# Performance work log

Measured on AMD Instinct MI355X. Metric: run time of the kernel, lower is better.

The kernel has to match this reference:

```python
import jax, jax.numpy as jnp
import numpy as np

B, Q, D = 262144, 25, 9  # batch, num_queries, key_value_size
SEGS = [(0, 3), (3, 13), (13, 23), (23, 25)]  # joint, object, goal, block token ranges
EPS = 1e-5


def setup_inputs() -> dict:
    key = jax.random.key(0)
    ks = jax.random.split(key, 17)
    inp = {"x": jax.random.normal(ks[0], (B, Q, D), dtype=jnp.float32)}
    names = ["W_jk", "b_jk", "W_ok", "b_ok", "W_gk", "b_gk", "W_bk", "b_bk",
             "W_jv", "b_jv", "W_ov", "b_ov", "W_gv", "b_gv", "W_bv", "b_bv"]
    scale = 1.0 / np.sqrt(D)  # torch Linear default init range
    for i, n in enumerate(names):
        shp = (D, D) if n.startswith("W") else (D,)
        inp[n] = jax.random.uniform(ks[i + 1], shp, jnp.float32, -scale, scale)
    inp["ln_g"] = jnp.ones((D,), jnp.float32)
    inp["ln_b"] = jnp.zeros((D,), jnp.float32)
    return inp


def reference(x, W_jk, b_jk, W_ok, b_ok, W_gk, b_gk, W_bk, b_bk,
              W_jv, b_jv, W_ov, b_ov, W_gv, b_gv, W_bv, b_bv, ln_g, ln_b):
    def proj(seg, W, b):
        s, e = seg  # [B, n, D] @ W.T + b  (torch Linear convention: W is [out,in])
        return jnp.einsum('bnd,kd->bnk', x[:, s:e], W) + b

    keys = jnp.concatenate([proj(SEGS[0], W_jk, b_jk), proj(SEGS[1], W_ok, b_ok),
                            proj(SEGS[2], W_gk, b_gk), proj(SEGS[3], W_bk, b_bk)], axis=1)
    values = jnp.concatenate([proj(SEGS[0], W_jv, b_jv), proj(SEGS[1], W_ov, b_ov),
                              proj(SEGS[2], W_gv, b_gv), proj(SEGS[3], W_bv, b_bv)], axis=1)
    # self-attention with queries == keys (as in the original forward)
    scores = jnp.einsum('bqd,bkd->bqk', keys, keys)  # [B, Q, Q]
    attn = jax.nn.softmax(scores, axis=-1)  # dropout = identity in eval
    res = jnp.einsum('bqk,bkd->bqd', attn, values)
    y = x + res
    mu = jnp.mean(y, axis=-1, keepdims=True)
    var = jnp.mean(jnp.square(y - mu), axis=-1, keepdims=True)
    return (y - mu) * jax.lax.rsqrt(var + EPS) * ln_g + ln_b
```

## Files before the change

### kernel.cpp

```cpp
#include <hip/hip_runtime.h>

#define TPB 256
#define BPB 64
#define NQ 25
#define ND 9
#define XWORDS (BPB * NQ * ND)
#define X4 (XWORDS / 4)
#define KV_OFF 8000
#define SMEM_WORDS 16000
#define SOFTMAX_SHIFT 40.0f

typedef _Float16 h2 __attribute__((ext_vector_type(2)));
typedef float f4 __attribute__((ext_vector_type(4)));

__device__ __forceinline__ float dot2acc(h2 a, h2 b, float c) {
#if __has_builtin(__builtin_amdgcn_fdot2)
    return __builtin_amdgcn_fdot2(a, b, c, false);
#else
    return c + (float)a[0] * (float)b[0] + (float)a[1] * (float)b[1];
#endif
}

__global__ __launch_bounds__(TPB, 2) void attn_fused(
    const float* __restrict__ x,
    const float* __restrict__ Wjk, const float* __restrict__ bjk,
    const float* __restrict__ Wok, const float* __restrict__ bok,
    const float* __restrict__ Wgk, const float* __restrict__ bgk,
    const float* __restrict__ Wbk, const float* __restrict__ bbk,
    const float* __restrict__ Wjv, const float* __restrict__ bjv,
    const float* __restrict__ Wov, const float* __restrict__ bov,
    const float* __restrict__ Wgv, const float* __restrict__ bgv,
    const float* __restrict__ Wbv, const float* __restrict__ bbv,
    const float* __restrict__ ln_g, const float* __restrict__ ln_b,
    float* __restrict__ out)
{
    __shared__ unsigned int sm[SMEM_WORDS];

    const int tid  = threadIdx.x;
    const int lane = tid & 63;
    const int w    = __builtin_amdgcn_readfirstlane(tid >> 6);
    const long base = (long)blockIdx.x * XWORDS;

    {
        const f4* src = (const f4*)(x + base);
        f4* dst = (f4*)sm;
        #pragma unroll
        for (int i = 0; i < 15; ++i) {
            int idx = tid + i * TPB;
            if (idx < X4) dst[idx] = src[idx];
        }
    }
    __syncthreads();

    const int qs = (w == 0) ? 0 : 6 * w + 1;
    const int qc = (w == 0) ? 7 : 6;

    float xr[7][9];
    #pragma unroll
    for (int j = 0; j < 7; ++j) {
        if (j < qc) {
            const float* xsrc = (const float*)sm + lane * (NQ * ND) + (qs + j) * ND;
            #pragma unroll
            for (int d = 0; d < ND; ++d) xr[j][d] = xsrc[d];
        }
    }
    __syncthreads();

    h2 kreg[7][5];
    #pragma unroll
    for (int j = 0; j < 7; ++j) {
        if (j < qc) {
            const int q = qs + j;
            const int seg = (q >= 3) + (q >= 13) + (q >= 23);
            const float* Wk = (seg == 0) ? Wjk : (seg == 1) ? Wok : (seg == 2) ? Wgk : Wbk;
            const float* bk = (seg == 0) ? bjk : (seg == 1) ? bok : (seg == 2) ? bgk : bbk;
            const float* Wv = (seg == 0) ? Wjv : (seg == 1) ? Wov : (seg == 2) ? Wgv : Wbv;
            const float* bv = (seg == 0) ? bjv : (seg == 1) ? bov : (seg == 2) ? bgv : bbv;

            float kk[9], vv[9];
            #pragma unroll
            for (int o = 0; o < ND; ++o) {
                float ak = bk[o];
                float av = bv[o];
                #pragma unroll
                for (int i = 0; i < ND; ++i) {
                    ak += Wk[o * ND + i] * xr[j][i];
                    av += Wv[o * ND + i] * xr[j][i];
                }
                kk[o] = ak; vv[o] = av;
            }
            #pragma unroll
            for (int hp = 0; hp < 5; ++hp) {
                float k0 = kk[2 * hp], k1 = (hp < 4) ? kk[2 * hp + 1] : 0.0f;
                float v0 = vv[2 * hp], v1 = (hp < 4) ? vv[2 * hp + 1] : 0.0f;
                h2 kh; kh[0] = (_Float16)k0; kh[1] = (_Float16)k1;
                h2 vh; vh[0] = (_Float16)v0; vh[1] = (_Float16)v1;
                kreg[j][hp] = kh;
                sm[hp * 1600 + q * 64 + lane]          = __builtin_bit_cast(unsigned int, kh);
                sm[KV_OFF + hp * 1600 + q * 64 + lane] = __builtin_bit_cast(unsigned int, vh);
            }
        }
    }
    __syncthreads();

    float res[7][9];
    float lsum[7];
    #pragma unroll
    for (int j = 0; j < 7; ++j) {
        lsum[j] = 0.0f;
        #pragma unroll
        for (int d = 0; d < ND; ++d) res[j][d] = 0.0f;
    }

    #pragma unroll 1
    for (int k = 0; k < NQ; ++k) {
        h2 kh[5], vh[5];
        #pragma unroll
        for (int hp = 0; hp < 5; ++hp) {
            kh[hp] = __builtin_bit_cast(h2, sm[hp * 1600 + k * 64 + lane]);
            vh[hp] = __builtin_bit_cast(h2, sm[KV_OFF + hp * 1600 + k * 64 + lane]);
        }
        float vf[9];
        #pragma unroll
        for (int hp = 0; hp < 4; ++hp) {
            vf[2 * hp]     = (float)vh[hp][0];
            vf[2 * hp + 1] = (float)vh[hp][1];
        }
        vf[8] = (float)vh[4][0];

        #pragma unroll
        for (int j = 0; j < 7; ++j) {
            if (j < qc) {
                float s = 0.0f;
                #pragma unroll
                for (int hp = 0; hp < 5; ++hp) s = dot2acc(kreg[j][hp], kh[hp], s);
                float e = __expf(s - SOFTMAX_SHIFT);
                lsum[j] += e;
                #pragma unroll
                for (int d = 0; d < ND; ++d) res[j][d] += e * vf[d];
            }
        }
    }
    __syncthreads();

    float g[9], bb[9];
    #pragma unroll
    for (int d = 0; d < ND; ++d) { g[d] = ln_g[d]; bb[d] = ln_b[d]; }

    #pragma unroll
    for (int j = 0; j < 7; ++j) {
        if (j < qc) {
            float rl = __builtin_amdgcn_rcpf(lsum[j]);
            float y[9];
            float s = 0.0f;
            #pragma unroll
            for (int d = 0; d < ND; ++d) {
                y[d] = xr[j][d] + res[j][d] * rl;
                s += y[d];
            }
            float mu = s * (1.0f / 9.0f);
            float var = 0.0f;
            #pragma unroll
            for (int d = 0; d < ND; ++d) {
                float t = y[d] - mu;
                var += t * t;
            }
            float rs = __builtin_amdgcn_rsqf(var * (1.0f / 9.0f) + 1e-5f);
            float* ydst = (float*)sm + lane * (NQ * ND) + (qs + j) * ND;
            #pragma unroll
            for (int d = 0; d < ND; ++d) ydst[d] = (y[d] - mu) * rs * g[d] + bb[d];
        }
    }
    __syncthreads();

    {
        const f4* srcs = (const f4*)sm;
        f4* dstg = (f4*)(out + base);
        #pragma unroll
        for (int i = 0; i < 15; ++i) {
            int idx = tid + i * TPB;
            if (idx < X4) dstg[idx] = srcs[idx];
        }
    }
}

extern "C" void kernel_launch(void* const* d_in, const int* in_sizes, int n_in,
                              void* d_out, int out_size, void* d_ws, size_t ws_size,
                              hipStream_t stream) {
    const float* x   = (const float*)d_in[0];
    const float* Wjk = (const float*)d_in[1];
    const float* bjk = (const float*)d_in[2];
    const float* Wok = (const float*)d_in[3];
    const float* bok = (const float*)d_in[4];
    const float* Wgk = (const float*)d_in[5];
    const float* bgk = (const float*)d_in[6];
    const float* Wbk = (const float*)d_in[7];
    const float* bbk = (const float*)d_in[8];
    const float* Wjv = (const float*)d_in[9];
    const float* bjv = (const float*)d_in[10];
    const float* Wov = (const float*)d_in[11];
    const float* bov = (const float*)d_in[12];
    const float* Wgv = (const float*)d_in[13];
    const float* bgv = (const float*)d_in[14];
    const float* Wbv = (const float*)d_in[15];
    const float* bbv = (const float*)d_in[16];
    const float* lng = (const float*)d_in[17];
    const float* lnb = (const float*)d_in[18];
    float* out = (float*)d_out;

    const int nbatch = in_sizes[0] / (NQ * ND);
    const int nblocks = nbatch / BPB;

    hipLaunchKernelGGL(attn_fused, dim3(nblocks), dim3(TPB), 0, stream,
                       x, Wjk, bjk, Wok, bok, Wgk, bgk, Wbk, bbk,
                       Wjv, bjv, Wov, bov, Wgv, bgv, Wbv, bbv, lng, lnb, out);
}
```

Measured before the change: 513.1 us.

## Use 512 threads per block, exp2 softmax, packed FMAs, nontemporal stores

Doubles the threads per block to 512 so each wave handles 3-4 queries instead of 6-7, which cuts per-thread register arrays and raises the occupancy target in launch bounds. Folds log2(e) into the fp16 query keys and the constant shift into the accumulator init, so the softmax uses a raw exp2. Accumulates values as float2 vectors to enable packed FMA, and writes output with nontemporal stores. The trade-offs are extra fp16 rounding from the scaled keys and more LDS reads of K/V per batch element across waves.

New measurement: 508.0 us. No clear change (-1.0%).

```diff
diff --git a/kernel.cpp b/kernel.cpp
--- a/kernel.cpp
+++ b/kernel.cpp
@@ -1,6 +1,6 @@
 #include <hip/hip_runtime.h>
 
-#define TPB 256
+#define TPB 512
 #define BPB 64
 #define NQ 25
 #define ND 9
@@ -8,9 +8,11 @@
 #define X4 (XWORDS / 4)
 #define KV_OFF 8000
 #define SMEM_WORDS 16000
-#define SOFTMAX_SHIFT 40.0f
+#define LOG2E 1.44269504088896340736f
+#define C2 (40.0f * LOG2E)
 
 typedef _Float16 h2 __attribute__((ext_vector_type(2)));
+typedef float f2 __attribute__((ext_vector_type(2)));
 typedef float f4 __attribute__((ext_vector_type(4)));
 
 __device__ __forceinline__ float dot2acc(h2 a, h2 b, float c) {
@@ -21,7 +23,15 @@
 #endif
 }
 
-__global__ __launch_bounds__(TPB, 2) void attn_fused(
+__device__ __forceinline__ float fast_exp2(float x) {
+#if __has_builtin(__builtin_amdgcn_exp2f)
+    return __builtin_amdgcn_exp2f(x);
+#else
+    return exp2f(x);
+#endif
+}
+
+__global__ __launch_bounds__(TPB, 4) void attn_fused(
     const float* __restrict__ x,
     const float* __restrict__ Wjk, const float* __restrict__ bjk,
     const float* __restrict__ Wok, const float* __restrict__ bok,
@@ -34,7 +44,7 @@
     const float* __restrict__ ln_g, const float* __restrict__ ln_b,
     float* __restrict__ out)
 {
-    __shared__ unsigned int sm[SMEM_WORDS];
+    __shared__ alignas(16) unsigned int sm[SMEM_WORDS];
 
     const int tid  = threadIdx.x;
     const int lane = tid & 63;
@@ -45,19 +55,19 @@
         const f4* src = (const f4*)(x + base);
         f4* dst = (f4*)sm;
         #pragma unroll
-        for (int i = 0; i < 15; ++i) {
+        for (int i = 0; i < 8; ++i) {
             int idx = tid + i * TPB;
             if (idx < X4) dst[idx] = src[idx];
         }
     }
     __syncthreads();
 
-    const int qs = (w == 0) ? 0 : 6 * w + 1;
-    const int qc = (w == 0) ? 7 : 6;
-
-    float xr[7][9];
-    #pragma unroll
-    for (int j = 0; j < 7; ++j) {
+    const int qs = (w == 0) ? 0 : 3 * w + 1;
+    const int qc = (w == 0) ? 4 : 3;
+
+    float xr[4][9];
+    #pragma unroll
+    for (int j = 0; j < 4; ++j) {
         if (j < qc) {
             const float* xsrc = (const float*)sm + lane * (NQ * ND) + (qs + j) * ND;
             #pragma unroll
@@ -66,9 +76,9 @@
     }
     __syncthreads();
 
-    h2 kreg[7][5];
-    #pragma unroll
-    for (int j = 0; j < 7; ++j) {
+    h2 kreg[4][5];
+    #pragma unroll
+    for (int j = 0; j < 4; ++j) {
         if (j < qc) {
             const int q = qs + j;
             const int seg = (q >= 3) + (q >= 13) + (q >= 23);
@@ -95,7 +105,8 @@
                 float v0 = vv[2 * hp], v1 = (hp < 4) ? vv[2 * hp + 1] : 0.0f;
                 h2 kh; kh[0] = (_Float16)k0; kh[1] = (_Float16)k1;
                 h2 vh; vh[0] = (_Float16)v0; vh[1] = (_Float16)v1;
-                kreg[j][hp] = kh;
+                h2 ks; ks[0] = (_Float16)(k0 * LOG2E); ks[1] = (_Float16)(k1 * LOG2E);
+                kreg[j][hp] = ks;
                 sm[hp * 1600 + q * 64 + lane]          = __builtin_bit_cast(unsigned int, kh);
                 sm[KV_OFF + hp * 1600 + q * 64 + lane] = __builtin_bit_cast(unsigned int, vh);
             }
@@ -103,13 +114,13 @@
     }
     __syncthreads();
 
-    float res[7][9];
-    float lsum[7];
-    #pragma unroll
-    for (int j = 0; j < 7; ++j) {
+    f2 res2[4][5];
+    float lsum[4];
+    #pragma unroll
+    for (int j = 0; j < 4; ++j) {
         lsum[j] = 0.0f;
         #pragma unroll
-        for (int d = 0; d < ND; ++d) res[j][d] = 0.0f;
+        for (int hp = 0; hp < 5; ++hp) { res2[j][hp][0] = 0.0f; res2[j][hp][1] = 0.0f; }
     }
 
     #pragma unroll 1
@@ -120,24 +131,24 @@
             kh[hp] = __builtin_bit_cast(h2, sm[hp * 1600 + k * 64 + lane]);
             vh[hp] = __builtin_bit_cast(h2, sm[KV_OFF + hp * 1600 + k * 64 + lane]);
         }
-        float vf[9];
-        #pragma unroll
-        for (int hp = 0; hp < 4; ++hp) {
-            vf[2 * hp]     = (float)vh[hp][0];
-            vf[2 * hp + 1] = (float)vh[hp][1];
-        }
-        vf[8] = (float)vh[4][0];
-
-        #pragma unroll
-        for (int j = 0; j < 7; ++j) {
+        f2 vf2[5];
+        #pragma unroll
+        for (int hp = 0; hp < 5; ++hp) {
+            vf2[hp][0] = (float)vh[hp][0];
+            vf2[hp][1] = (float)vh[hp][1];
+        }
+
+        #pragma unroll
+        for (int j = 0; j < 4; ++j) {
             if (j < qc) {
-                float s = 0.0f;
+                float s = -C2;
                 #pragma unroll
                 for (int hp = 0; hp < 5; ++hp) s = dot2acc(kreg[j][hp], kh[hp], s);
-                float e = __expf(s - SOFTMAX_SHIFT);
+                float e = fast_exp2(s);
                 lsum[j] += e;
+                f2 e2; e2[0] = e; e2[1] = e;
                 #pragma unroll
-                for (int d = 0; d < ND; ++d) res[j][d] += e * vf[d];
+                for (int hp = 0; hp < 5; ++hp) res2[j][hp] += e2 * vf2[hp];
             }
         }
     }
@@ -148,14 +159,22 @@
     for (int d = 0; d < ND; ++d) { g[d] = ln_g[d]; bb[d] = ln_b[d]; }
 
     #pragma unroll
-    for (int j = 0; j < 7; ++j) {
+    for (int j = 0; j < 4; ++j) {
         if (j < qc) {
+            float res[9];
+            #pragma unroll
+            for (int hp = 0; hp < 4; ++hp) {
+                res[2 * hp]     = res2[j][hp][0];
+                res[2 * hp + 1] = res2[j][hp][1];
+            }
+            res[8] = res2[j][4][0];
+
             float rl = __builtin_amdgcn_rcpf(lsum[j]);
             float y[9];
             float s = 0.0f;
             #pragma unroll
             for (int d = 0; d < ND; ++d) {
-                y[d] = xr[j][d] + res[j][d] * rl;
+                y[d] = xr[j][d] + res[d] * rl;
                 s += y[d];
             }
             float mu = s * (1.0f / 9.0f);
@@ -177,9 +196,9 @@
         const f4* srcs = (const f4*)sm;
         f4* dstg = (f4*)(out + base);
         #pragma unroll
-        for (int i = 0; i < 15; ++i) {
+        for (int i = 0; i < 8; ++i) {
             int idx = tid + i * TPB;
-            if (idx < X4) dstg[idx] = srcs[idx];
+            if (idx < X4) __builtin_nontemporal_store(srcs[idx], &dstg[idx]);
         }
     }
 }
```
